# Optimization experiments

Hardware: AMD Instinct MI355X
Metric: run time of the kernel (lower is better)

## Reference

```python
import jax, jax.numpy as jnp
from jax import lax
import numpy as np

EPS = 1e-5  # BatchNorm eps; eval-mode BN with running_mean=0, running_var=1


def _conv(x, w, b):
    return lax.conv_general_dilated(x, w, (1, 1), 'SAME', dimension_numbers=('NCHW', 'OIHW', 'NCHW')) + b[None, :, None, None]


def _cbr(x, w, b, g, a):
    # Conv -> BN(eval, mean=0, var=1) -> ReLU
    y = _conv(x, w, b)
    y = g[None, :, None, None] * (y * (1.0 / np.sqrt(1.0 + EPS))) + a[None, :, None, None]
    return jax.nn.relu(y)


def _pool(x):
    return lax.reduce_window(x, -jnp.inf, lax.max, (1, 1, 2, 2), (1, 1, 2, 2), 'VALID')


def _up2(x):
    B, C, H, W = x.shape
    Ho, Wo = 2 * H, 2 * W
    ys = jnp.arange(Ho) * ((H - 1) / (Ho - 1))
    xs = jnp.arange(Wo) * ((W - 1) / (Wo - 1))
    y0 = jnp.floor(ys).astype(jnp.int32); y1 = jnp.minimum(y0 + 1, H - 1)
    x0 = jnp.floor(xs).astype(jnp.int32); x1 = jnp.minimum(x0 + 1, W - 1)
    wy = (ys - y0).astype(x.dtype); wx = (xs - x0).astype(x.dtype)
    row = x[:, :, y0, :] * (1 - wy)[None, None, :, None] + x[:, :, y1, :] * wy[None, None, :, None]
    return row[:, :, :, x0] * (1 - wx) + row[:, :, :, x1] * wx


def _fcas(x, w, b):
    # FullyConnectedAtomicSpace: for each interior pixel (i,j) of x[0,1],
    # p = #(channel > v), n = #(channel == v), e = #(channel < v), out = (p*w0+b0 + n*w1+b1 + e*w2+b2)/3.
    # Vectorized via sort + searchsorted: O(N log N) instead of O(N^2).
    ch = x[0, 1]
    H, W = ch.shape
    flat = ch.ravel(); N = flat.size
    s = jnp.sort(flat)
    left = jnp.searchsorted(s, flat, side='left')
    right = jnp.searchsorted(s, flat, side='right')
    e = left.astype(x.dtype)            # count <
    n = (right - left).astype(x.dtype)  # count ==
    p = (N - right).astype(x.dtype)     # count >
    val = ((p * w[0] + b[0] + n * w[1] + b[1] + e * w[2] + b[2]) / 3.0).reshape(H, W)
    ii = jnp.arange(H); jj = jnp.arange(W)
    interior = ((ii >= 1) & (ii <= H - 2))[:, None] & ((jj >= 1) & (jj <= W - 2))[None, :]
    new_ch = jnp.where(interior, val, ch)
    # original converts to numpy and back -> detaches the whole tensor
    return lax.stop_gradient(x.at[0, 1].set(new_ch))


def _forward(x, w_inc, b_inc, g_inc, a_inc, w_d1, b_d1, g_d1, a_d1, w_d2, b_d2, g_d2, a_d2,
             w_d3, b_d3, g_d3, a_d3, w_u2, b_u2, g_u2, a_u2, w_u3, b_u3, g_u3, a_u3,
             w_u4, b_u4, g_u4, a_u4, w_out, b_out, fcas_w, fcas_b):
    x1 = _cbr(x, w_inc, b_inc, g_inc, a_inc)            # [B,8,512,512]
    x2 = _cbr(_pool(x1), w_d1, b_d1, g_d1, a_d1)        # [B,16,256,256]
    x3 = _cbr(_pool(x2), w_d2, b_d2, g_d2, a_d2)        # [B,32,128,128]
    x4 = _cbr(_pool(x3), w_d3, b_d3, g_d3, a_d3)        # [B,32,64,64]
    x4 = _fcas(x4, fcas_w, fcas_b)
    u = _cbr(jnp.concatenate([x3, _up2(x4)], axis=1), w_u2, b_u2, g_u2, a_u2)  # 64->16
    u = _cbr(jnp.concatenate([x2, _up2(u)], axis=1), w_u3, b_u3, g_u3, a_u3)   # 32->8
    u = _cbr(jnp.concatenate([x1, _up2(u)], axis=1), w_u4, b_u4, g_u4, a_u4)   # 16->4
    return jax.nn.sigmoid(_conv(u, w_out, b_out))       # [B,1,512,512]


def setup_inputs():
    key = jax.random.key(0)
    ks = jax.random.split(key, 24)
    d = {}
    d['x'] = jax.random.normal(ks[0], (8, 3, 512, 512), jnp.float32)
    specs = [('inc', 8, 3), ('d1', 16, 8), ('d2', 32, 16), ('d3', 32, 32), ('u2', 16, 64), ('u3', 8, 32), ('u4', 4, 16)]
    for idx, (nm, o, i) in enumerate(specs):
        k1, k2, k3, k4 = jax.random.split(ks[idx + 1], 4)
        d['w_' + nm] = jax.random.normal(k1, (o, i, 3, 3), jnp.float32) * 0.1
        d['b_' + nm] = jax.random.normal(k2, (o,), jnp.float32) * 0.1
        d['g_' + nm] = 1.0 + jax.random.normal(k3, (o,), jnp.float32) * 0.1
        d['a_' + nm] = jax.random.normal(k4, (o,), jnp.float32) * 0.1
    d['w_out'] = jax.random.normal(ks[20], (1, 4, 1, 1), jnp.float32) * 0.1
    d['b_out'] = jax.random.normal(ks[21], (1,), jnp.float32) * 0.1
    d['fcas_w'] = jnp.array([0.5, 0.5, 0.5], jnp.float32)
    d['fcas_b'] = jnp.array([0.5, 0.5, 0.5], jnp.float32)
    return d


def reference(x, w_inc, b_inc, g_inc, a_inc, w_d1, b_d1, g_d1, a_d1, w_d2, b_d2, g_d2, a_d2,
              w_d3, b_d3, g_d3, a_d3, w_u2, b_u2, g_u2, a_u2, w_u3, b_u3, g_u3, a_u3,
              w_u4, b_u4, g_u4, a_u4, w_out, b_out, fcas_w, fcas_b):
    return _forward(x, w_inc, b_inc, g_inc, a_inc, w_d1, b_d1, g_d1, a_d1, w_d2, b_d2, g_d2, a_d2,
                    w_d3, b_d3, g_d3, a_d3, w_u2, b_u2, g_u2, a_u2, w_u3, b_u3, g_u3, a_u3,
                    w_u4, b_u4, g_u4, a_u4, w_out, b_out, fcas_w, fcas_b)
```

## Files before the change

kernel.cpp:

```cpp
#include <hip/hip_runtime.h>
#include <hip/hip_bf16.h>

#define BN_RSQ 0.9999950000374997f

struct LayerP {
  const float* w; const float* b; const float* g; const float* a;
  float* wf; float* bf; int cout; int cin;
};
struct AllP { LayerP L[7]; float* zbuf; };

__global__ void prefold_kernel(AllP A) {
  LayerP p = A.L[blockIdx.y];
  int n = p.cout * p.cin * 9;
  int i = blockIdx.x * 256 + threadIdx.x;
  if (i < n) {
    int o = i / (p.cin * 9);
    p.wf[i] = p.w[i] * p.g[o] * BN_RSQ;
  }
  if (i < p.cout) p.bf[i] = p.b[i] * p.g[i] * BN_RSQ + p.a[i];
  if (blockIdx.y == 0 && blockIdx.x == 0 && i < 16) A.zbuf[i] = 0.f;
}

__device__ __forceinline__ void async_row_f32(const float* g, float* l) {
  __builtin_amdgcn_global_load_lds(
      (const __attribute__((address_space(1))) void*)g,
      (__attribute__((address_space(3))) void*)l, 4, 0, 0);
}

__global__ void up2_kernel(const float* __restrict__ in, float* __restrict__ out,
                           int Hi, int Wi) {
  const int Ho = 2 * Hi, Wo = 2 * Wi;
  const int ox = blockIdx.x * 16 + threadIdx.x;
  const int oy = blockIdx.y * 16 + threadIdx.y;
  const int bc = blockIdx.z;
  const float sy = (float)(Hi - 1) / (float)(Ho - 1);
  const float sx = (float)(Wi - 1) / (float)(Wo - 1);
  float fy = oy * sy, fx = ox * sx;
  int y0 = (int)floorf(fy); int y1 = min(y0 + 1, Hi - 1);
  int x0 = (int)floorf(fx); int x1 = min(x0 + 1, Wi - 1);
  float wy = fy - (float)y0, wx = fx - (float)x0;
  const float* p = in + (size_t)bc * Hi * Wi;
  float a00 = p[y0 * Wi + x0], a01 = p[y0 * Wi + x1];
  float a10 = p[y1 * Wi + x0], a11 = p[y1 * Wi + x1];
  float r0 = a00 * (1.f - wy) + a10 * wy;
  float r1 = a01 * (1.f - wy) + a11 * wy;
  out[((size_t)bc * Ho + oy) * Wo + ox] = r0 * (1.f - wx) + r1 * wx;
}

template <int CIN1, int CIN2, int COUTG, int OSPLIT, bool WRITE_POOL>
__launch_bounds__(256)
__global__ void conv3x3_direct(const float* __restrict__ in1,
                               const float* __restrict__ in2,
                               const float* __restrict__ wf,
                               const float* __restrict__ bf,
                               const float* __restrict__ zbuf,
                               float* __restrict__ out,
                               float* __restrict__ pout, int H, int W) {
  constexpr int CIN = CIN1 + CIN2;
  constexpr int COUT = COUTG * OSPLIT;
  __shared__ float wsm[COUTG * CIN * 12];

  const int tid = threadIdx.x;
  const int txp = (tid & 15) * 4;
  const int ty = tid >> 4;
  const int gx0 = blockIdx.x * 64;
  const int gy0 = blockIdx.y * 16;
  const int b = blockIdx.z & 7;
  const int og = blockIdx.z >> 3;
  const int obase = og * COUTG;
  const int lane = tid & 63;

  for (int idx = tid; idx < COUTG * CIN * 9; idx += 256) {
    int o = idx / (CIN * 9);
    int r = idx - o * (CIN * 9);
    int c = r / 9;
    int t = r - c * 9;
    wsm[(o * CIN + c) * 12 + t] = wf[((obase + o) * CIN + c) * 9 + t];
  }
  __syncthreads();

  const int ox = gx0 + txp;
  const int oy = gy0 + ty;
  const bool vM = (oy >= 1);
  const bool vP = (oy + 1 < H);
  const float selL = (ox >= 1) ? 1.f : 0.f;
  const float selR = (ox + 4 < W) ? 1.f : 0.f;
  const float* zp = zbuf + 4 - (size_t)ox;

  float acc[COUTG][4];
#pragma unroll
  for (int o = 0; o < COUTG; ++o)
#pragma unroll
    for (int i = 0; i < 4; ++i) acc[o][i] = 0.f;

  auto body = [&](const float* __restrict__ plane, int cabs) {
    const float* rC = plane + (size_t)oy * W;
    const float* rM = vM ? (rC - W) : zp;
    const float* rP = vP ? (rC + W) : zp;
    float rr[3][6];
#pragma unroll
    for (int dy = 0; dy < 3; ++dy) {
      const float* p = (dy == 0 ? rM : (dy == 1 ? rC : rP)) + ox;
      float4 v4 = *(const float4*)p;
      float lm = p[-1];
      float rp = p[4];
      rr[dy][0] = lm * selL;
      rr[dy][1] = v4.x; rr[dy][2] = v4.y; rr[dy][3] = v4.z; rr[dy][4] = v4.w;
      rr[dy][5] = rp * selR;
    }
#pragma unroll
    for (int o = 0; o < COUTG; ++o) {
      const float4* wp = (const float4*)&wsm[(o * CIN + cabs) * 12];
      float4 wa = wp[0];
      float4 wb = wp[1];
      float w8 = wsm[(o * CIN + cabs) * 12 + 8];
#pragma unroll
      for (int i = 0; i < 4; ++i) {
        float s = acc[o][i];
        s = fmaf(rr[0][i + 0], wa.x, s);
        s = fmaf(rr[0][i + 1], wa.y, s);
        s = fmaf(rr[0][i + 2], wa.z, s);
        s = fmaf(rr[1][i + 0], wa.w, s);
        s = fmaf(rr[1][i + 1], wb.x, s);
        s = fmaf(rr[1][i + 2], wb.y, s);
        s = fmaf(rr[2][i + 0], wb.z, s);
        s = fmaf(rr[2][i + 1], wb.w, s);
        s = fmaf(rr[2][i + 2], w8, s);
        acc[o][i] = s;
      }
    }
  };

#pragma unroll 1
  for (int c = 0; c < CIN1; ++c)
    body(in1 + (size_t)(b * CIN1 + c) * H * W, c);
  if (CIN2 > 0) {
#pragma unroll 1
    for (int c = 0; c < CIN2; ++c)
      body(in2 + (size_t)(b * CIN2 + c) * H * W, CIN1 + c);
  }

  const int H2 = H >> 1, W2 = W >> 1;
#pragma unroll
  for (int o = 0; o < COUTG; ++o) {
    float bo = bf[obase + o];
    float rv[4];
#pragma unroll
    for (int i = 0; i < 4; ++i) rv[i] = fmaxf(acc[o][i] + bo, 0.f);
    *(float4*)&out[((size_t)(b * COUT + obase + o) * H + oy) * W + ox] =
        *(float4*)rv;
    if (WRITE_POOL) {
      float m0 = fmaxf(rv[0], rv[1]);
      float m1 = fmaxf(rv[2], rv[3]);
      float q0 = fmaxf(m0, __shfl_down(m0, 16));
      float q1 = fmaxf(m1, __shfl_down(m1, 16));
      if (((lane >> 4) & 1) == 0) {
        float2 pw; pw.x = q0; pw.y = q1;
        *(float2*)&pout[((size_t)(b * COUT + obase + o) * H2 + (oy >> 1)) * W2 +
                        (ox >> 1)] = pw;
      }
    }
  }
}

template <int CIN1, int CIN2, int COUTG, int OSPLIT, bool UP_IN2, bool FUSE_OUT,
          bool WRITE_POOL>
__launch_bounds__(256)
__global__ void conv3x3_cbr(const float* __restrict__ in1,
                            const float* __restrict__ in2,
                            const float* __restrict__ wf,
                            const float* __restrict__ bf,
                            const float* __restrict__ wout,
                            const float* __restrict__ bout,
                            float* __restrict__ out,
                            float* __restrict__ pout, int H, int W) {
  constexpr int CIN = CIN1 + CIN2;
  constexpr int COUT = COUTG * OSPLIT;
  constexpr int PPT = 4;
  constexpr int CHUNK = (CIN < 4) ? CIN : 4;
  constexpr int XS = 68;
  constexpr int YT = 18;
  constexpr int ROWS = CHUNK * YT;

  __shared__ float tile[CHUNK][YT][XS];
  __shared__ float wsm[COUTG * CIN * 12];

  const int tid = threadIdx.x;
  const int txp = (tid & 15) * PPT;
  const int ty = tid >> 4;
  const int gx0 = blockIdx.x * 64;
  const int gy0 = blockIdx.y * 16;
  const int b = blockIdx.z & 7;
  const int og = blockIdx.z >> 3;
  const int obase = og * COUTG;

  const int lane = tid & 63;
  const int wv = tid >> 6;

  const int Hi = H >> 1, Wi = W >> 1;
  const float syf = UP_IN2 ? (float)(Hi - 1) / (float)(H - 1) : 0.f;

  int ux0 = 0, ux1 = 0;
  float uwx = 0.f;
  if (UP_IN2) {
    const float sx = (float)(Wi - 1) / (float)(W - 1);
    float fx = (gx0 + lane) * sx;
    ux0 = (int)fx;
    ux1 = min(ux0 + 1, Wi - 1);
    uwx = fx - (float)ux0;
  }

  for (int idx = tid; idx < COUTG * CIN * 9; idx += 256) {
    int o = idx / (CIN * 9);
    int r = idx - o * (CIN * 9);
    int c = r / 9;
    int t = r - c * 9;
    wsm[(o * CIN + c) * 12 + t] = wf[((obase + o) * CIN + c) * 9 + t];
  }

  float acc[COUTG][PPT];
#pragma unroll
  for (int o = 0; o < COUTG; ++o)
#pragma unroll
    for (int i = 0; i < PPT; ++i) acc[o][i] = 0.f;

  for (int cc = 0; cc < CIN; cc += CHUNK) {
    __syncthreads();
    if (wv < CHUNK) {
      const int c = wv;
      const int cg = cc + c;
      const bool dir1 = (CIN2 == 0 || cg < CIN1);
      if (dir1 || !UP_IN2) {
        const float* src;
        int cb;
        if (dir1) { src = in1; cb = b * CIN1 + cg; }
        else      { src = in2; cb = b * CIN2 + (cg - CIN1); }
        const float* base =
            src + (size_t)cb * H * W + (size_t)(gy0 - 1) * W + gx0 + lane;
#pragma unroll
        for (int yy = 0; yy < YT; ++yy) {
          const int iy = gy0 + yy - 1;
          if (iy >= 0 && iy < H) {
            async_row_f32(base + (size_t)yy * W, &tile[c][yy][1]);
          } else {
            tile[c][yy][1 + lane] = 0.f;
          }
        }
      } else {
        const int cb = b * CIN2 + (cg - CIN1);
#pragma unroll 1
        for (int yy = 0; yy < YT; ++yy) {
          const int iy = gy0 + yy - 1;
          float v = 0.f;
          if (iy >= 0 && iy < H) {
            float fy = iy * syf;
            int y0 = (int)fy;
            int y1 = min(y0 + 1, Hi - 1);
            float wy = fy - (float)y0;
            const float* r0p = in2 + (size_t)(cb * Hi + y0) * Wi;
            const float* r1p = in2 + (size_t)(cb * Hi + y1) * Wi;
            float a00 = r0p[ux0], a01 = r0p[ux1];
            float a10 = r1p[ux0], a11 = r1p[ux1];
            float r0 = a00 * (1.f - wy) + a10 * wy;
            float r1 = a01 * (1.f - wy) + a11 * wy;
            v = r0 * (1.f - uwx) + r1 * uwx;
          }
          tile[c][yy][1 + lane] = v;
        }
      }
    }
    for (int idx = tid; idx < 2 * ROWS; idx += 256) {
      const int row = idx >> 1;
      const int side = idx & 1;
      const int c = row / YT;
      const int yy = row - c * YT;
      const int iy = gy0 + yy - 1;
      const int ix = side ? (gx0 + 64) : (gx0 - 1);
      const int cg = cc + c;
      float v = 0.f;
      if (iy >= 0 && iy < H && ix >= 0 && ix < W) {
        if (CIN2 == 0 || cg < CIN1) {
          const int cb = b * CIN1 + cg;
          v = in1[(size_t)(cb * H + iy) * W + ix];
        } else if (UP_IN2) {
          const int cb = b * CIN2 + (cg - CIN1);
          const float sx = (float)(Wi - 1) / (float)(W - 1);
          float fy = iy * syf, fx = ix * sx;
          int y0 = (int)fy; int y1 = min(y0 + 1, Hi - 1);
          int x0 = (int)fx; int x1 = min(x0 + 1, Wi - 1);
          float wy = fy - (float)y0, wx = fx - (float)x0;
          const float* p = in2 + (size_t)cb * Hi * Wi;
          float a00 = p[y0 * Wi + x0], a01 = p[y0 * Wi + x1];
          float a10 = p[y1 * Wi + x0], a11 = p[y1 * Wi + x1];
          float r0 = a00 * (1.f - wy) + a10 * wy;
          float r1 = a01 * (1.f - wy) + a11 * wy;
          v = r0 * (1.f - wx) + r1 * wx;
        } else {
          const int cb = b * CIN2 + (cg - CIN1);
          v = in2[(size_t)(cb * H + iy) * W + ix];
        }
      }
      tile[c][yy][side ? 65 : 0] = v;
    }
    __syncthreads();
#pragma unroll
    for (int c = 0; c < CHUNK; ++c) {
      float rr[3][6];
#pragma unroll
      for (int dy = 0; dy < 3; ++dy) {
        const float* p = &tile[c][ty + dy][txp];
        float4 a4 = *(const float4*)p;
        float2 b2 = *(const float2*)(p + 4);
        rr[dy][0] = a4.x; rr[dy][1] = a4.y; rr[dy][2] = a4.z; rr[dy][3] = a4.w;
        rr[dy][4] = b2.x; rr[dy][5] = b2.y;
      }
      const int cabs = cc + c;
#pragma unroll
      for (int o = 0; o < COUTG; ++o) {
        const float4* wp = (const float4*)&wsm[(o * CIN + cabs) * 12];
        float4 wa = wp[0];
        float4 wb = wp[1];
        float w8 = wsm[(o * CIN + cabs) * 12 + 8];
#pragma unroll
        for (int i = 0; i < PPT; ++i) {
          float s = acc[o][i];
          s = fmaf(rr[0][i + 0], wa.x, s);
          s = fmaf(rr[0][i + 1], wa.y, s);
          s = fmaf(rr[0][i + 2], wa.z, s);
          s = fmaf(rr[1][i + 0], wa.w, s);
          s = fmaf(rr[1][i + 1], wb.x, s);
          s = fmaf(rr[1][i + 2], wb.y, s);
          s = fmaf(rr[2][i + 0], wb.z, s);
          s = fmaf(rr[2][i + 1], wb.w, s);
          s = fmaf(rr[2][i + 2], w8, s);
          acc[o][i] = s;
        }
      }
    }
  }

  const int oy = gy0 + ty;
  const int ox = gx0 + txp;
  if (FUSE_OUT) {
    float sv[PPT];
#pragma unroll
    for (int i = 0; i < PPT; ++i) sv[i] = bout[0];
#pragma unroll
    for (int o = 0; o < COUTG; ++o) {
      float bo = bf[obase + o], wo = wout[o];
#pragma unroll
      for (int i = 0; i < PPT; ++i) {
        float rr2 = fmaxf(acc[o][i] + bo, 0.f);
        sv[i] = fmaf(rr2, wo, sv[i]);
      }
    }
#pragma unroll
    for (int i = 0; i < PPT; ++i) sv[i] = 1.f / (1.f + __expf(-sv[i]));
    *(float4*)&out[((size_t)b * H + oy) * W + ox] = *(float4*)sv;
  } else {
    const int H2 = H >> 1, W2 = W >> 1;
#pragma unroll
    for (int o = 0; o < COUTG; ++o) {
      float bo = bf[obase + o];
      float rv[PPT];
#pragma unroll
      for (int i = 0; i < PPT; ++i) rv[i] = fmaxf(acc[o][i] + bo, 0.f);
      *(float4*)&out[((size_t)(b * COUT + obase + o) * H + oy) * W + ox] =
          *(float4*)rv;
      if (WRITE_POOL) {
        float m0 = fmaxf(rv[0], rv[1]);
        float m1 = fmaxf(rv[2], rv[3]);
        float q0 = fmaxf(m0, __shfl_down(m0, 16));
        float q1 = fmaxf(m1, __shfl_down(m1, 16));
        if (((lane >> 4) & 1) == 0) {
          float2 pw; pw.x = q0; pw.y = q1;
          *(float2*)&pout[((size_t)(b * COUT + obase + o) * H2 + (oy >> 1)) * W2 +
                          (ox >> 1)] = pw;
        }
      }
    }
  }
}

__global__ void fcas_partial(const float* __restrict__ ch,
                             int* __restrict__ pcnt, int* __restrict__ ncnt) {
  __shared__ float sv[256];
  const int e = blockIdx.x * 256 + threadIdx.x;
  const int s = blockIdx.y;
  sv[threadIdx.x] = ch[s * 256 + threadIdx.x];
  __syncthreads();
  const float v = ch[e];
  int p = 0, n = 0;
#pragma unroll 4
  for (int k = 0; k < 256; ++k) {
    float u = sv[k];
    p += (u > v);
    n += (u == v);
  }
  pcnt[s * 4096 + e] = p;
  ncnt[s * 4096 + e] = n;
}

__global__ void fcas_final(float* __restrict__ ch,
                           const int* __restrict__ pcnt,
                           const int* __restrict__ ncnt,
                           const float* __restrict__ w,
                           const float* __restrict__ bb) {
  const int e = blockIdx.x * 256 + threadIdx.x;
  int p = 0, n = 0;
#pragma unroll
  for (int s = 0; s < 16; ++s) {
    p += pcnt[s * 4096 + e];
    n += ncnt[s * 4096 + e];
  }
  const int el = 4096 - p - n;
  float val = ((float)p * w[0] + bb[0] + (float)n * w[1] + bb[1] +
               (float)el * w[2] + bb[2]) / 3.0f;
  int i = e >> 6, j = e & 63;
  bool interior = (i >= 1) && (i <= 62) && (j >= 1) && (j <= 62);
  if (interior) ch[e] = val;
}

extern "C" void kernel_launch(void* const* d_in, const int* in_sizes, int n_in,
                              void* d_out, int out_size, void* d_ws, size_t ws_size,
                              hipStream_t stream) {
  const float* x      = (const float*)d_in[0];
  const float* w_inc  = (const float*)d_in[1];
  const float* b_inc  = (const float*)d_in[2];
  const float* g_inc  = (const float*)d_in[3];
  const float* a_inc  = (const float*)d_in[4];
  const float* w_d1   = (const float*)d_in[5];
  const float* b_d1   = (const float*)d_in[6];
  const float* g_d1   = (const float*)d_in[7];
  const float* a_d1   = (const float*)d_in[8];
  const float* w_d2   = (const float*)d_in[9];
  const float* b_d2   = (const float*)d_in[10];
  const float* g_d2   = (const float*)d_in[11];
  const float* a_d2   = (const float*)d_in[12];
  const float* w_d3   = (const float*)d_in[13];
  const float* b_d3   = (const float*)d_in[14];
  const float* g_d3   = (const float*)d_in[15];
  const float* a_d3   = (const float*)d_in[16];
  const float* w_u2   = (const float*)d_in[17];
  const float* b_u2   = (const float*)d_in[18];
  const float* g_u2   = (const float*)d_in[19];
  const float* a_u2   = (const float*)d_in[20];
  const float* w_u3   = (const float*)d_in[21];
  const float* b_u3   = (const float*)d_in[22];
  const float* g_u3   = (const float*)d_in[23];
  const float* a_u3   = (const float*)d_in[24];
  const float* w_u4   = (const float*)d_in[25];
  const float* b_u4   = (const float*)d_in[26];
  const float* g_u4   = (const float*)d_in[27];
  const float* a_u4   = (const float*)d_in[28];
  const float* w_out  = (const float*)d_in[29];
  const float* b_out  = (const float*)d_in[30];
  const float* fcas_w = (const float*)d_in[31];
  const float* fcas_b = (const float*)d_in[32];

  float* ws = (float*)d_ws;
  float* x1  = ws;
  float* p1  = x1 + 16777216;
  float* x2  = p1 + 4194304;
  float* p2  = x2 + 8388608;
  float* x3  = p2 + 2097152;
  float* p3  = x3 + 4194304;
  float* x4  = p3 + 1048576;
  float* upa = x4 + 1048576;
  float* uo2 = upa + 4194304;
  float* uo3 = uo2 + 2097152;
  int*   pcnt = (int*)(uo3 + 4194304);
  int*   ncnt = pcnt + 65536;
  float* upb = x3;
  float* wfp = (float*)(ncnt + 65536);
  float* wf_inc = wfp;
  float* wf_d1  = wf_inc + 216;
  float* wf_d2  = wf_d1 + 1152;
  float* wf_d3  = wf_d2 + 4608;
  float* wf_u2  = wf_d3 + 9216;
  float* wf_u3  = wf_u2 + 9216;
  float* wf_u4  = wf_u3 + 2304;
  float* bf_inc = wf_u4 + 576;
  float* bf_d1  = bf_inc + 8;
  float* bf_d2  = bf_d1 + 16;
  float* bf_d3  = bf_d2 + 32;
  float* bf_u2  = bf_d3 + 32;
  float* bf_u3  = bf_u2 + 16;
  float* bf_u4  = bf_u3 + 8;
  float* zbuf   = bf_u4 + 4;
  float* outp = (float*)d_out;

  AllP A;
  A.L[0] = {w_inc, b_inc, g_inc, a_inc, wf_inc, bf_inc, 8, 3};
  A.L[1] = {w_d1, b_d1, g_d1, a_d1, wf_d1, bf_d1, 16, 8};
  A.L[2] = {w_d2, b_d2, g_d2, a_d2, wf_d2, bf_d2, 32, 16};
  A.L[3] = {w_d3, b_d3, g_d3, a_d3, wf_d3, bf_d3, 32, 32};
  A.L[4] = {w_u2, b_u2, g_u2, a_u2, wf_u2, bf_u2, 16, 64};
  A.L[5] = {w_u3, b_u3, g_u3, a_u3, wf_u3, bf_u3, 8, 32};
  A.L[6] = {w_u4, b_u4, g_u4, a_u4, wf_u4, bf_u4, 4, 16};
  A.zbuf = zbuf;
  prefold_kernel<<<dim3(36, 7), dim3(256), 0, stream>>>(A);

  dim3 blk(256);
  dim3 blk2(16, 16);

  conv3x3_cbr<3, 0, 8, 1, false, false, true><<<dim3(8, 32, 8), blk, 0, stream>>>(
      x, nullptr, wf_inc, bf_inc, nullptr, nullptr, x1, p1, 512, 512);
  conv3x3_direct<8, 0, 4, 4, true><<<dim3(4, 16, 32), blk, 0, stream>>>(
      p1, nullptr, wf_d1, bf_d1, zbuf, x2, p2, 256, 256);
  conv3x3_direct<16, 0, 4, 8, true><<<dim3(2, 8, 64), blk, 0, stream>>>(
      p2, nullptr, wf_d2, bf_d2, zbuf, x3, p3, 128, 128);
  conv3x3_direct<32, 0, 2, 16, false><<<dim3(1, 4, 128), blk, 0, stream>>>(
      p3, nullptr, wf_d3, bf_d3, zbuf, x4, nullptr, 64, 64);
  fcas_partial<<<dim3(16, 16), blk, 0, stream>>>(x4 + 4096, pcnt, ncnt);
  fcas_final<<<dim3(16), blk, 0, stream>>>(x4 + 4096, pcnt, ncnt, fcas_w, fcas_b);
  up2_kernel<<<dim3(8, 8, 256), blk2, 0, stream>>>(x4, upa, 64, 64);
  conv3x3_direct<32, 32, 2, 8, false><<<dim3(2, 8, 64), blk, 0, stream>>>(
      x3, upa, wf_u2, bf_u2, zbuf, uo2, nullptr, 128, 128);
  up2_kernel<<<dim3(16, 16, 128), blk2, 0, stream>>>(uo2, upb, 128, 128);
  conv3x3_direct<16, 16, 2, 4, false><<<dim3(4, 16, 32), blk, 0, stream>>>(
      x2, upb, wf_u3, bf_u3, zbuf, uo3, nullptr, 256, 256);
  conv3x3_cbr<8, 8, 4, 1, true, true, false><<<dim3(8, 32, 8), blk, 0, stream>>>(
      x1, uo3, wf_u4, bf_u4, w_out, b_out, outp, nullptr, 512, 512);
}
```

Measured before the change: 490.4 us.

## Add specialized final up-conv kernel with LDS upsample tile and direct skip reads

Replaces the generic templated conv for the last decoder layer with a dedicated kernel. Per block it computes the bilinear-upsampled channels once into an LDS tile with halo, and reads the skip-connection input directly from global memory with register sliding windows. The output 1x1 conv and sigmoid are fused into the epilogue. The workspace is reordered so the small weight and count buffers come first, which risks alignment side effects for the large tensors.

```diff
diff --git a/kernel.cpp b/kernel.cpp
--- a/kernel.cpp
+++ b/kernel.cpp
@@ -161,6 +161,202 @@
       }
     }
   }
+}
+
+__launch_bounds__(256)
+__global__ void conv3x3_u4(const float* __restrict__ in1,
+                           const float* __restrict__ in2,
+                           const float* __restrict__ wf,
+                           const float* __restrict__ bf,
+                           const float* __restrict__ wout,
+                           const float* __restrict__ bout,
+                           const float* __restrict__ zbuf,
+                           float* __restrict__ out) {
+  constexpr int H = 512, W = 512, Hi = 256, Wi = 256;
+  constexpr int CIN1 = 8, CIN2 = 8, CIN = 16, COUT = 4;
+  __shared__ float utile[CIN2][18][68];
+  __shared__ float wsm[COUT * CIN * 12];
+
+  const int tid = threadIdx.x;
+  const int lane = tid & 63;
+  const int wv = tid >> 6;
+  const int txp = (tid & 15) * 4;
+  const int ty = tid >> 4;
+  const int gx0 = blockIdx.x * 64;
+  const int gy0 = blockIdx.y * 16;
+  const int b = blockIdx.z;
+
+  for (int idx = tid; idx < COUT * CIN * 9; idx += 256) {
+    int o = idx / (CIN * 9);
+    int r = idx - o * (CIN * 9);
+    int c = r / 9;
+    int t = r - c * 9;
+    wsm[(o * CIN + c) * 12 + t] = wf[(o * CIN + c) * 9 + t];
+  }
+
+  const float sx = (float)(Wi - 1) / (float)(W - 1);
+  const float sy = (float)(Hi - 1) / (float)(H - 1);
+  const float* in2b = in2 + (size_t)b * CIN2 * Hi * Wi;
+
+  {
+    const int gox = gx0 + lane;
+    const float fx = gox * sx;
+    const int x0 = (int)fx;
+    const int x1i = min(x0 + 1, Wi - 1);
+    const float wx = fx - (float)x0;
+    for (int t5 = wv; t5 < CIN2 * 18; t5 += 4) {
+      const int c = t5 / 18;
+      const int yy = t5 - c * 18;
+      const int goy = gy0 + yy - 1;
+      float v = 0.f;
+      if (goy >= 0 && goy < H) {
+        const float fy = goy * sy;
+        const int y0 = (int)fy;
+        const int y1 = min(y0 + 1, Hi - 1);
+        const float wy = fy - (float)y0;
+        const float* p0 = in2b + ((size_t)c * Hi + y0) * Wi;
+        const float* p1 = in2b + ((size_t)c * Hi + y1) * Wi;
+        float a00 = p0[x0], a01 = p0[x1i];
+        float a10 = p1[x0], a11 = p1[x1i];
+        float r0 = a00 * (1.f - wy) + a10 * wy;
+        float r1 = a01 * (1.f - wy) + a11 * wy;
+        v = r0 * (1.f - wx) + r1 * wx;
+      }
+      utile[c][yy][1 + lane] = v;
+    }
+  }
+  for (int i = tid; i < 2 * CIN2 * 18; i += 256) {
+    const int side = i & 1;
+    const int row = i >> 1;
+    const int c = row / 18;
+    const int yy = row - c * 18;
+    const int gox = side ? (gx0 + 64) : (gx0 - 1);
+    const int goy = gy0 + yy - 1;
+    float v = 0.f;
+    if (goy >= 0 && goy < H && gox >= 0 && gox < W) {
+      const float fy = goy * sy;
+      const float fx = gox * sx;
+      const int y0 = (int)fy;
+      const int y1 = min(y0 + 1, Hi - 1);
+      const int x0 = (int)fx;
+      const int x1i = min(x0 + 1, Wi - 1);
+      const float wy = fy - (float)y0;
+      const float wx = fx - (float)x0;
+      const float* p = in2b + (size_t)c * Hi * Wi;
+      float a00 = p[y0 * Wi + x0], a01 = p[y0 * Wi + x1i];
+      float a10 = p[y1 * Wi + x0], a11 = p[y1 * Wi + x1i];
+      float r0 = a00 * (1.f - wy) + a10 * wy;
+      float r1 = a01 * (1.f - wy) + a11 * wy;
+      v = r0 * (1.f - wx) + r1 * wx;
+    }
+    utile[c][yy][side ? 65 : 0] = v;
+  }
+  __syncthreads();
+
+  const int ox = gx0 + txp;
+  const int oy = gy0 + ty;
+  const bool vM = (oy >= 1);
+  const bool vP = (oy + 1 < H);
+  const float selL = (ox >= 1) ? 1.f : 0.f;
+  const float selR = (ox + 4 < W) ? 1.f : 0.f;
+  const float* zp = zbuf + 4 - (size_t)ox;
+
+  float acc[COUT][4];
+#pragma unroll
+  for (int o = 0; o < COUT; ++o)
+#pragma unroll
+    for (int i = 0; i < 4; ++i) acc[o][i] = 0.f;
+
+#pragma unroll 1
+  for (int c = 0; c < CIN1; ++c) {
+    const float* plane = in1 + (size_t)(b * CIN1 + c) * H * W;
+    const float* rC = plane + (size_t)oy * W;
+    const float* rM = vM ? (rC - W) : zp;
+    const float* rP = vP ? (rC + W) : zp;
+    float rr[3][6];
+#pragma unroll
+    for (int dy = 0; dy < 3; ++dy) {
+      const float* p = (dy == 0 ? rM : (dy == 1 ? rC : rP)) + ox;
+      float4 v4 = *(const float4*)p;
+      float lm = p[-1];
+      float rp = p[4];
+      rr[dy][0] = lm * selL;
+      rr[dy][1] = v4.x; rr[dy][2] = v4.y; rr[dy][3] = v4.z; rr[dy][4] = v4.w;
+      rr[dy][5] = rp * selR;
+    }
+#pragma unroll
+    for (int o = 0; o < COUT; ++o) {
+      const float4* wp = (const float4*)&wsm[(o * CIN + c) * 12];
+      float4 wa = wp[0];
+      float4 wb = wp[1];
+      float w8 = wsm[(o * CIN + c) * 12 + 8];
+#pragma unroll
+      for (int i = 0; i < 4; ++i) {
+        float s = acc[o][i];
+        s = fmaf(rr[0][i + 0], wa.x, s);
+        s = fmaf(rr[0][i + 1], wa.y, s);
+        s = fmaf(rr[0][i + 2], wa.z, s);
+        s = fmaf(rr[1][i + 0], wa.w, s);
+        s = fmaf(rr[1][i + 1], wb.x, s);
+        s = fmaf(rr[1][i + 2], wb.y, s);
+        s = fmaf(rr[2][i + 0], wb.z, s);
+        s = fmaf(rr[2][i + 1], wb.w, s);
+        s = fmaf(rr[2][i + 2], w8, s);
+        acc[o][i] = s;
+      }
+    }
+  }
+
+#pragma unroll
+  for (int c = 0; c < CIN2; ++c) {
+    float rr[3][6];
+#pragma unroll
+    for (int dy = 0; dy < 3; ++dy) {
+      const float* p = &utile[c][ty + dy][txp];
+      float4 a4 = *(const float4*)p;
+      float2 b2 = *(const float2*)(p + 4);
+      rr[dy][0] = a4.x; rr[dy][1] = a4.y; rr[dy][2] = a4.z; rr[dy][3] = a4.w;
+      rr[dy][4] = b2.x; rr[dy][5] = b2.y;
+    }
+    const int cabs = CIN1 + c;
+#pragma unroll
+    for (int o = 0; o < COUT; ++o) {
+      const float4* wp = (const float4*)&wsm[(o * CIN + cabs) * 12];
+      float4 wa = wp[0];
+      float4 wb = wp[1];
+      float w8 = wsm[(o * CIN + cabs) * 12 + 8];
+#pragma unroll
+      for (int i = 0; i < 4; ++i) {
+        float s = acc[o][i];
+        s = fmaf(rr[0][i + 0], wa.x, s);
+        s = fmaf(rr[0][i + 1], wa.y, s);
+        s = fmaf(rr[0][i + 2], wa.z, s);
+        s = fmaf(rr[1][i + 0], wa.w, s);
+        s = fmaf(rr[1][i + 1], wb.x, s);
+        s = fmaf(rr[1][i + 2], wb.y, s);
+        s = fmaf(rr[2][i + 0], wb.z, s);
+        s = fmaf(rr[2][i + 1], wb.w, s);
+        s = fmaf(rr[2][i + 2], w8, s);
+        acc[o][i] = s;
+      }
+    }
+  }
+
+  float sv[4];
+#pragma unroll
+  for (int i = 0; i < 4; ++i) sv[i] = bout[0];
+#pragma unroll
+  for (int o = 0; o < COUT; ++o) {
+    float bo = bf[o], wo = wout[o];
+#pragma unroll
+    for (int i = 0; i < 4; ++i) {
+      float rr2 = fmaxf(acc[o][i] + bo, 0.f);
+      sv[i] = fmaf(rr2, wo, sv[i]);
+    }
+  }
+#pragma unroll
+  for (int i = 0; i < 4; ++i) sv[i] = 1.f / (1.f + __expf(-sv[i]));
+  *(float4*)&out[((size_t)b * H + oy) * W + ox] = *(float4*)sv;
 }
 
 template <int CIN1, int CIN2, int COUTG, int OSPLIT, bool UP_IN2, bool FUSE_OUT,
@@ -459,21 +655,8 @@
   const float* fcas_b = (const float*)d_in[32];
 
   float* ws = (float*)d_ws;
-  float* x1  = ws;
-  float* p1  = x1 + 16777216;
-  float* x2  = p1 + 4194304;
-  float* p2  = x2 + 8388608;
-  float* x3  = p2 + 2097152;
-  float* p3  = x3 + 4194304;
-  float* x4  = p3 + 1048576;
-  float* upa = x4 + 1048576;
-  float* uo2 = upa + 4194304;
-  float* uo3 = uo2 + 2097152;
-  int*   pcnt = (int*)(uo3 + 4194304);
-  int*   ncnt = pcnt + 65536;
-  float* upb = x3;
-  float* wfp = (float*)(ncnt + 65536);
-  float* wf_inc = wfp;
+  float* zbuf   = ws;
+  float* wf_inc = ws + 16;
   float* wf_d1  = wf_inc + 216;
   float* wf_d2  = wf_d1 + 1152;
   float* wf_d3  = wf_d2 + 4608;
@@ -487,7 +670,19 @@
   float* bf_u2  = bf_d3 + 32;
   float* bf_u3  = bf_u2 + 16;
   float* bf_u4  = bf_u3 + 8;
-  float* zbuf   = bf_u4 + 4;
+  int*   pcnt   = (int*)(ws + 27424);
+  int*   ncnt   = pcnt + 65536;
+  float* x1  = (float*)(ncnt + 65536);
+  float* p1  = x1 + 16777216;
+  float* x2  = p1 + 4194304;
+  float* p2  = x2 + 8388608;
+  float* x3  = p2 + 2097152;
+  float* p3  = x3 + 4194304;
+  float* x4  = p3 + 1048576;
+  float* upa = x4 + 1048576;
+  float* uo2 = upa + 4194304;
+  float* uo3 = uo2 + 2097152;
+  float* upb = x3;
   float* outp = (float*)d_out;
 
   AllP A;
@@ -520,6 +715,6 @@
   up2_kernel<<<dim3(16, 16, 128), blk2, 0, stream>>>(uo2, upb, 128, 128);
   conv3x3_direct<16, 16, 2, 4, false><<<dim3(4, 16, 32), blk, 0, stream>>>(
       x2, upb, wf_u3, bf_u3, zbuf, uo3, nullptr, 256, 256);
-  conv3x3_cbr<8, 8, 4, 1, true, true, false><<<dim3(8, 32, 8), blk, 0, stream>>>(
-      x1, uo3, wf_u4, bf_u4, w_out, b_out, outp, nullptr, 512, 512);
-}
+  conv3x3_u4<<<dim3(8, 32, 8), blk, 0, stream>>>(
+      x1, uo3, wf_u4, bf_u4, w_out, b_out, zbuf, outp);
+}
```

Result: no change. 484.5 us (-1.2%).

## Split final upsample from last conv and retune decoder output-channel grouping

Applied to the files above, without the earlier changes.

The final stage no longer does the bilinear upsample inside the LDS-tiled conv kernel. It materialises the upsampled tensor with a separate up2 kernel into the freed p1 buffer, then runs a new direct-load conv kernel that applies the 1x1 output projection and sigmoid in its epilogue. The decoder convs u2 and u3 now group four output channels per block instead of two, halving the grid's channel splits. The blockIdx.z decode becomes generic in OSPLIT, and the workspace is reordered so that small buffers come first. This trades an extra full-resolution write and read for simpler conv indexing and more input reuse per block.

```diff
diff --git a/kernel.cpp b/kernel.cpp
--- a/kernel.cpp
+++ b/kernel.cpp
@@ -65,8 +65,8 @@
   const int ty = tid >> 4;
   const int gx0 = blockIdx.x * 64;
   const int gy0 = blockIdx.y * 16;
-  const int b = blockIdx.z & 7;
-  const int og = blockIdx.z >> 3;
+  const int og = blockIdx.z % OSPLIT;
+  const int b = blockIdx.z / OSPLIT;
   const int obase = og * COUTG;
   const int lane = tid & 63;
 
@@ -161,6 +161,110 @@
       }
     }
   }
+}
+
+__launch_bounds__(256)
+__global__ void conv3x3_u4d(const float* __restrict__ in1,
+                            const float* __restrict__ in2,
+                            const float* __restrict__ wf,
+                            const float* __restrict__ bf,
+                            const float* __restrict__ wout,
+                            const float* __restrict__ bout,
+                            const float* __restrict__ zbuf,
+                            float* __restrict__ out) {
+  constexpr int H = 512, W = 512, CIN1 = 8, CIN2 = 8, CIN = 16, COUT = 4;
+  __shared__ float wsm[COUT * CIN * 12];
+
+  const int tid = threadIdx.x;
+  const int txp = (tid & 15) * 4;
+  const int ty = tid >> 4;
+  const int gx0 = blockIdx.x * 64;
+  const int gy0 = blockIdx.y * 16;
+  const int b = blockIdx.z;
+
+  for (int idx = tid; idx < COUT * CIN * 9; idx += 256) {
+    int o = idx / (CIN * 9);
+    int r = idx - o * (CIN * 9);
+    int c = r / 9;
+    int t = r - c * 9;
+    wsm[(o * CIN + c) * 12 + t] = wf[(o * CIN + c) * 9 + t];
+  }
+  __syncthreads();
+
+  const int ox = gx0 + txp;
+  const int oy = gy0 + ty;
+  const bool vM = (oy >= 1);
+  const bool vP = (oy + 1 < H);
+  const float selL = (ox >= 1) ? 1.f : 0.f;
+  const float selR = (ox + 4 < W) ? 1.f : 0.f;
+  const float* zp = zbuf + 4 - (size_t)ox;
+
+  float acc[COUT][4];
+#pragma unroll
+  for (int o = 0; o < COUT; ++o)
+#pragma unroll
+    for (int i = 0; i < 4; ++i) acc[o][i] = 0.f;
+
+  auto body = [&](const float* __restrict__ plane, int cabs) {
+    const float* rC = plane + (size_t)oy * W;
+    const float* rM = vM ? (rC - W) : zp;
+    const float* rP = vP ? (rC + W) : zp;
+    float rr[3][6];
+#pragma unroll
+    for (int dy = 0; dy < 3; ++dy) {
+      const float* p = (dy == 0 ? rM : (dy == 1 ? rC : rP)) + ox;
+      float4 v4 = *(const float4*)p;
+      float lm = p[-1];
+      float rp = p[4];
+      rr[dy][0] = lm * selL;
+      rr[dy][1] = v4.x; rr[dy][2] = v4.y; rr[dy][3] = v4.z; rr[dy][4] = v4.w;
+      rr[dy][5] = rp * selR;
+    }
+#pragma unroll
+    for (int o = 0; o < COUT; ++o) {
+      const float4* wp = (const float4*)&wsm[(o * CIN + cabs) * 12];
+      float4 wa = wp[0];
+      float4 wb = wp[1];
+      float w8 = wsm[(o * CIN + cabs) * 12 + 8];
+#pragma unroll
+      for (int i = 0; i < 4; ++i) {
+        float s = acc[o][i];
+        s = fmaf(rr[0][i + 0], wa.x, s);
+        s = fmaf(rr[0][i + 1], wa.y, s);
+        s = fmaf(rr[0][i + 2], wa.z, s);
+        s = fmaf(rr[1][i + 0], wa.w, s);
+        s = fmaf(rr[1][i + 1], wb.x, s);
+        s = fmaf(rr[1][i + 2], wb.y, s);
+        s = fmaf(rr[2][i + 0], wb.z, s);
+        s = fmaf(rr[2][i + 1], wb.w, s);
+        s = fmaf(rr[2][i + 2], w8, s);
+        acc[o][i] = s;
+      }
+    }
+  };
+
+#pragma unroll 1
+  for (int c = 0; c < CIN1; ++c)
+    body(in1 + (size_t)(b * CIN1 + c) * H * W, c);
+#pragma unroll 1
+  for (int c = 0; c < CIN2; ++c)
+    body(in2 + (size_t)(b * CIN2 + c) * H * W, CIN1 + c);
+
+  float sv[4];
+#pragma unroll
+  for (int i = 0; i < 4; ++i) sv[i] = bout[0];
+#pragma unroll
+  for (int o = 0; o < COUT; ++o) {
+    float bo = bf[o], wo = wout[o];
+#pragma unroll
+    for (int i = 0; i < 4; ++i) {
+      float rr2 = fmaxf(acc[o][i] + bo, 0.f);
+      sv[i] = fmaf(rr2, wo, sv[i]);
+    }
+  }
+#pragma unroll
+  for (int i = 0; i < 4; ++i) sv[i] = 1.f / (1.f + __expf(-sv[i]));
+  *(float4*)&out[((size_t)b * H + oy) * W + ox] = *(float4*)sv;
 }
 
 template <int CIN1, int CIN2, int COUTG, int OSPLIT, bool UP_IN2, bool FUSE_OUT,
@@ -459,21 +563,8 @@
   const float* fcas_b = (const float*)d_in[32];
 
   float* ws = (float*)d_ws;
-  float* x1  = ws;
-  float* p1  = x1 + 16777216;
-  float* x2  = p1 + 4194304;
-  float* p2  = x2 + 8388608;
-  float* x3  = p2 + 2097152;
-  float* p3  = x3 + 4194304;
-  float* x4  = p3 + 1048576;
-  float* upa = x4 + 1048576;
-  float* uo2 = upa + 4194304;
-  float* uo3 = uo2 + 2097152;
-  int*   pcnt = (int*)(uo3 + 4194304);
-  int*   ncnt = pcnt + 65536;
-  float* upb = x3;
-  float* wfp = (float*)(ncnt + 65536);
-  float* wf_inc = wfp;
+  float* zbuf   = ws;
+  float* wf_inc = ws + 16;
   float* wf_d1  = wf_inc + 216;
   float* wf_d2  = wf_d1 + 1152;
   float* wf_d3  = wf_d2 + 4608;
@@ -487,7 +578,20 @@
   float* bf_u2  = bf_d3 + 32;
   float* bf_u3  = bf_u2 + 16;
   float* bf_u4  = bf_u3 + 8;
-  float* zbuf   = bf_u4 + 4;
+  int*   pcnt   = (int*)(ws + 27424);
+  int*   ncnt   = pcnt + 65536;
+  float* x1  = (float*)(ncnt + 65536);
+  float* p1  = x1 + 16777216;
+  float* x2  = p1 + 4194304;
+  float* p2  = x2 + 8388608;
+  float* x3  = p2 + 2097152;
+  float* p3  = x3 + 4194304;
+  float* x4  = p3 + 1048576;
+  float* upa = x4 + 1048576;
+  float* uo2 = upa + 4194304;
+  float* uo3 = uo2 + 2097152;
+  float* upb = x3;
+  float* upx = p1;
   float* outp = (float*)d_out;
 
   AllP A;
@@ -515,11 +619,12 @@
   fcas_partial<<<dim3(16, 16), blk, 0, stream>>>(x4 + 4096, pcnt, ncnt);
   fcas_final<<<dim3(16), blk, 0, stream>>>(x4 + 4096, pcnt, ncnt, fcas_w, fcas_b);
   up2_kernel<<<dim3(8, 8, 256), blk2, 0, stream>>>(x4, upa, 64, 64);
-  conv3x3_direct<32, 32, 2, 8, false><<<dim3(2, 8, 64), blk, 0, stream>>>(
+  conv3x3_direct<32, 32, 4, 4, false><<<dim3(2, 8, 32), blk, 0, stream>>>(
       x3, upa, wf_u2, bf_u2, zbuf, uo2, nullptr, 128, 128);
   up2_kernel<<<dim3(16, 16, 128), blk2, 0, stream>>>(uo2, upb, 128, 128);
-  conv3x3_direct<16, 16, 2, 4, false><<<dim3(4, 16, 32), blk, 0, stream>>>(
+  conv3x3_direct<16, 16, 4, 2, false><<<dim3(4, 16, 16), blk, 0, stream>>>(
       x2, upb, wf_u3, bf_u3, zbuf, uo3, nullptr, 256, 256);
-  conv3x3_cbr<8, 8, 4, 1, true, true, false><<<dim3(8, 32, 8), blk, 0, stream>>>(
-      x1, uo3, wf_u4, bf_u4, w_out, b_out, outp, nullptr, 512, 512);
-}
+  up2_kernel<<<dim3(32, 32, 64), blk2, 0, stream>>>(uo3, upx, 256, 256);
+  conv3x3_u4d<<<dim3(8, 32, 8), blk, 0, stream>>>(
+      x1, upx, wf_u4, bf_u4, w_out, b_out, zbuf, outp);
+}
```

Measured after the change: 461.6 us. 5.9% less time.
